# Kernel optimization log

Measured on AMD Instinct MI355X. Metric: run time of the kernel, lower is better.

Reference implementation:

```python
import jax, jax.numpy as jnp
import numpy as np


def _cdist(x, y):
    # Euclidean (p=2) pairwise distances, matching torch.cdist.
    # x: [B, N, D], y: [B, M, D] -> [B, N, M]
    xx = jnp.sum(x * x, axis=-1)                      # [B, N]
    yy = jnp.sum(y * y, axis=-1)                      # [B, M]
    zz = jnp.einsum('bnd,bmd->bnm', x, y)             # [B, N, M]
    d2 = xx[:, :, None] + yy[:, None, :] - 2.0 * zz
    return jnp.sqrt(jnp.maximum(d2, 0.0))


def setup_inputs() -> dict:
    key = jax.random.key(0)
    k1, k2 = jax.random.split(key)
    gts = jax.random.normal(k1, (4, 8192, 3), dtype=jnp.float32)
    preds = jax.random.normal(k2, (4, 8192, 3), dtype=jnp.float32)
    return {"gts": gts, "preds": preds}


def reference(gts, preds):
    P = _cdist(gts, preds)                 # [B, N, M]
    loss_1 = jnp.sum(jnp.min(P, axis=1), axis=1)  # min over gts points, sum over preds
    loss_2 = jnp.sum(jnp.min(P, axis=2), axis=1)  # min over preds points, sum over gts
    return loss_1 + loss_2                 # [B]
```

## Files before the change

kernel.cpp:

```cpp
#include <hip/hip_runtime.h>
#include <math.h>

#define BB 4
#define NPTS 8192
#define THREADS 512
#define NQ_TOTAL (2 * BB * NPTS)
#define QBLK 256
#define QPWV 32
#define CHUNK 2048
#define NCHUNK (NPTS / CHUNK)
#define NFRAG (CHUNK / 32)
#define GLDS_PER_WAVE (CHUNK / 8 / 64)
#define FBLK (2 * BB * (NPTS / QBLK))

typedef __attribute__((ext_vector_type(8)))  short bf16x8;
typedef __attribute__((ext_vector_type(16))) float f32x16;


__device__ __forceinline__ unsigned short f2bf(float f) {
    unsigned u = __float_as_uint(f);
    u += 0x7FFF + ((u >> 16) & 1);
    return (unsigned short)(u >> 16);
}
__device__ __forceinline__ float bf2f(unsigned short h) {
    return __uint_as_float(((unsigned)h) << 16);
}

__global__ __launch_bounds__(256) void pack_kernel(
    const float* __restrict__ gts, const float* __restrict__ preds,
    uint4* __restrict__ refpack, uint4* __restrict__ qpack,
    float* __restrict__ out) {
    int idx = blockIdx.x * 256 + threadIdx.x;
    if (idx < BB) out[idx] = 0.0f;
    if (idx >= NQ_TOTAL) return;
    int set  = idx / (BB * NPTS);
    int pidx = idx - set * (BB * NPTS);
    const float* src = set ? preds : gts;
    unsigned short hx = f2bf(src[pidx * 3 + 0]);
    unsigned short hy = f2bf(src[pidx * 3 + 1]);
    unsigned short hz = f2bf(src[pidx * 3 + 2]);
    float fx = bf2f(hx), fy = bf2f(hy), fz = bf2f(hz);
    float rr = fmaf(fx, fx, fmaf(fy, fy, fz * fz));
    unsigned short hrr = f2bf(rr);
    unsigned short hlo = f2bf(rr - bf2f(hrr));
    const unsigned short ONE = 0x3F80;

    uint4 rv;
    rv.x = (unsigned)hx  | ((unsigned)hy  << 16);
    rv.y = (unsigned)hz  | ((unsigned)hrr << 16);
    rv.z = (unsigned)hlo | ((unsigned)ONE << 16);
    rv.w = (unsigned)ONE;
    refpack[idx] = rv;

    unsigned short nx = f2bf(-2.0f * fx);
    unsigned short ny = f2bf(-2.0f * fy);
    unsigned short nz = f2bf(-2.0f * fz);
    uint4 qv;
    qv.x = (unsigned)nx  | ((unsigned)ny  << 16);
    qv.y = (unsigned)nz  | ((unsigned)ONE << 16);
    qv.z = (unsigned)ONE | ((unsigned)hrr << 16);
    qv.w = (unsigned)hlo;
    qpack[idx] = qv;
}

#define FOLD8(P)                                                   \
    c0 = fminf(fminf((P)[0],  (P)[1]),  c0);                       \
    c1 = fminf(fminf((P)[2],  (P)[3]),  c1);                       \
    c2 = fminf(fminf((P)[4],  (P)[5]),  c2);                       \
    c3 = fminf(fminf((P)[6],  (P)[7]),  c3);                       \
    c0 = fminf(fminf((P)[8],  (P)[9]),  c0);                       \
    c1 = fminf(fminf((P)[10], (P)[11]), c1);                       \
    c2 = fminf(fminf((P)[12], (P)[13]), c2);                       \
    c3 = fminf(fminf((P)[14], (P)[15]), c3);

#define STEP(AQ, FN, DO_LOAD)                                               \
    {                                                                       \
        f32x16 dn = __builtin_amdgcn_mfma_f32_32x32x16_bf16(AQ, bq, zc, 0, 0, 0); \
        if (DO_LOAD) AQ = sp[(FN) * 32 + l31];                              \
        FOLD8(pp);                                                          \
        pp = pc; pc = dn;                                                   \
    }

#define STAGE(BUF, CBASE)                                                   \
    _Pragma("unroll")                                                       \
    for (int i = 0; i < GLDS_PER_WAVE; ++i)                                 \
        __builtin_amdgcn_global_load_lds(                                   \
            (const unsigned*)(rgl + (CBASE) + wid * 256 + i * 64 + lane),   \
            (unsigned*)&sref[BUF][wid * 256 + i * 64], 16, 0, 0);

__global__ __launch_bounds__(THREADS, 2) void chamfer_kernel(
    const uint4* __restrict__ refpack, const uint4* __restrict__ qpack,
    float* __restrict__ out) {
    __shared__ uint4 sref[2][CHUNK];

    int tid  = threadIdx.x;
    int blk  = blockIdx.x;
    int dir  = blk >> 7;
    int b    = (blk >> 5) & 3;
    int qg   = blk & 31;
    int rset = dir;
    int qset = dir ^ 1;
    int wid  = tid >> 6;
    int lane = tid & 63;
    int l31  = lane & 31;

    const uint4* rgl = refpack + (size_t)(rset * BB + b) * NPTS;

    STAGE(0, 0);

    size_t qoff = (size_t)(qset * BB + b) * NPTS + (size_t)qg * QBLK
                + (size_t)wid * QPWV;
    bf16x8 bq = {0, 0, 0, 0, 0, 0, 0, 0};
    if (lane < 32) bq = ((const bf16x8*)qpack)[qoff + l31];
    __syncthreads();

    f32x16 zc;
    #pragma unroll
    for (int r = 0; r < 16; ++r) zc[r] = 0.0f;

    float c0 = 3.0e38f, c1 = 3.0e38f, c2 = 3.0e38f, c3 = 3.0e38f;

    for (int c = 0; c < NCHUNK; ++c) {
        if (c + 1 < NCHUNK) {
            STAGE((c + 1) & 1, (c + 1) * CHUNK);
        }

        const bf16x8* sp = (const bf16x8*)sref[c & 1];

        bf16x8 a0 = sp[0 * 32 + l31];
        bf16x8 a1 = sp[1 * 32 + l31];
        bf16x8 a2 = sp[2 * 32 + l31];
        bf16x8 a3 = sp[3 * 32 + l31];
        bf16x8 a4 = sp[4 * 32 + l31];
        bf16x8 a5 = sp[5 * 32 + l31];
        bf16x8 a6 = sp[6 * 32 + l31];
        bf16x8 a7 = sp[7 * 32 + l31];

        f32x16 pp, pc;
        #pragma unroll
        for (int r = 0; r < 16; ++r) { pp[r] = 3.0e38f; pc[r] = 3.0e38f; }

        #pragma unroll
        for (int m = 0; m < NFRAG / 8; ++m) {
            const bool L = (m < NFRAG / 8 - 1);
            STEP(a0, (m + 1) * 8 + 0, L);
            STEP(a1, (m + 1) * 8 + 1, L);
            STEP(a2, (m + 1) * 8 + 2, L);
            STEP(a3, (m + 1) * 8 + 3, L);
            STEP(a4, (m + 1) * 8 + 4, L);
            STEP(a5, (m + 1) * 8 + 5, L);
            STEP(a6, (m + 1) * 8 + 6, L);
            STEP(a7, (m + 1) * 8 + 7, L);
        }
        FOLD8(pp);
        FOLD8(pc);

        __syncthreads();
    }

    float m = fminf(fminf(c0, c1), fminf(c2, c3));
    m = fminf(m, __shfl_xor(m, 32, 64));

    float d = 0.0f;
    if (lane < 32) d = sqrtf(fmaxf(m, 0.0f));
    #pragma unroll
    for (int off = 16; off > 0; off >>= 1)
        d += __shfl_down(d, off, 64);

    float* wsf = (float*)&sref[0][0];
    if (lane == 0) wsf[wid] = d;
    __syncthreads();
    if (tid == 0) {
        float s = wsf[0] + wsf[1] + wsf[2] + wsf[3]
                + wsf[4] + wsf[5] + wsf[6] + wsf[7];
        atomicAdd(out + b, s);
    }
}

extern "C" void kernel_launch(void* const* d_in, const int* in_sizes, int n_in,
                              void* d_out, int out_size, void* d_ws, size_t ws_size,
                              hipStream_t stream) {
    const float* gts   = (const float*)d_in[0];
    const float* preds = (const float*)d_in[1];
    float* out = (float*)d_out;

    char* ws = (char*)d_ws;
    uint4* refpack = (uint4*)ws;
    uint4* qpack   = (uint4*)(ws + (size_t)NQ_TOTAL * 16);

    pack_kernel<<<NQ_TOTAL / 256, 256, 0, stream>>>(
        gts, preds, refpack, qpack, out);

    chamfer_kernel<<<FBLK, THREADS, 0, stream>>>(refpack, qpack, out);
}
```

Before: 72.50 us.

## Split reference set in halves, double queries per wave, merge mins atomically

Each wave now handles 64 queries with two B fragments, so every A fragment loaded from LDS feeds two MFMAs, which halves the LDS reads per MFMA. The reference set is split into two halves across blocks, keeping the grid at 256 blocks. Partial minimum distances go to a workspace through atomicMin on the uint bit pattern, and a new merge kernel takes square roots and sums them. This costs an extra kernel launch, global atomics and more register pressure from the doubled accumulators.

```diff
diff --git a/kernel.cpp b/kernel.cpp
--- a/kernel.cpp
+++ b/kernel.cpp
@@ -5,13 +5,14 @@
 #define NPTS 8192
 #define THREADS 512
 #define NQ_TOTAL (2 * BB * NPTS)
-#define QBLK 256
-#define QPWV 32
+#define QBLK 512
+#define QPWV 64
+#define HALFN 4096
 #define CHUNK 2048
-#define NCHUNK (NPTS / CHUNK)
+#define NCHUNK (HALFN / CHUNK)
 #define NFRAG (CHUNK / 32)
 #define GLDS_PER_WAVE (CHUNK / 8 / 64)
-#define FBLK (2 * BB * (NPTS / QBLK))
+#define FBLK 256
 
 typedef __attribute__((ext_vector_type(8)))  short bf16x8;
 typedef __attribute__((ext_vector_type(16))) float f32x16;
@@ -29,10 +30,11 @@
 __global__ __launch_bounds__(256) void pack_kernel(
     const float* __restrict__ gts, const float* __restrict__ preds,
     uint4* __restrict__ refpack, uint4* __restrict__ qpack,
-    float* __restrict__ out) {
+    unsigned* __restrict__ minpart, float* __restrict__ out) {
     int idx = blockIdx.x * 256 + threadIdx.x;
     if (idx < BB) out[idx] = 0.0f;
     if (idx >= NQ_TOTAL) return;
+    minpart[idx] = 0x7F7FFFFFu;
     int set  = idx / (BB * NPTS);
     int pidx = idx - set * (BB * NPTS);
     const float* src = set ? preds : gts;
@@ -63,22 +65,25 @@
     qpack[idx] = qv;
 }
 
-#define FOLD8(P)                                                   \
-    c0 = fminf(fminf((P)[0],  (P)[1]),  c0);                       \
-    c1 = fminf(fminf((P)[2],  (P)[3]),  c1);                       \
-    c2 = fminf(fminf((P)[4],  (P)[5]),  c2);                       \
-    c3 = fminf(fminf((P)[6],  (P)[7]),  c3);                       \
-    c0 = fminf(fminf((P)[8],  (P)[9]),  c0);                       \
-    c1 = fminf(fminf((P)[10], (P)[11]), c1);                       \
-    c2 = fminf(fminf((P)[12], (P)[13]), c2);                       \
-    c3 = fminf(fminf((P)[14], (P)[15]), c3);
-
-#define STEP(AQ, FN, DO_LOAD)                                               \
+#define FOLD8(P, X0, X1, X2, X3)                                   \
+    X0 = fminf(fminf((P)[0],  (P)[1]),  X0);                       \
+    X1 = fminf(fminf((P)[2],  (P)[3]),  X1);                       \
+    X2 = fminf(fminf((P)[4],  (P)[5]),  X2);                       \
+    X3 = fminf(fminf((P)[6],  (P)[7]),  X3);                       \
+    X0 = fminf(fminf((P)[8],  (P)[9]),  X0);                       \
+    X1 = fminf(fminf((P)[10], (P)[11]), X1);                       \
+    X2 = fminf(fminf((P)[12], (P)[13]), X2);                       \
+    X3 = fminf(fminf((P)[14], (P)[15]), X3);
+
+#define STEP2(AQ, FN, DO_LOAD)                                              \
     {                                                                       \
-        f32x16 dn = __builtin_amdgcn_mfma_f32_32x32x16_bf16(AQ, bq, zc, 0, 0, 0); \
+        f32x16 dn0 = __builtin_amdgcn_mfma_f32_32x32x16_bf16(AQ, bq0, zc, 0, 0, 0); \
+        f32x16 dn1 = __builtin_amdgcn_mfma_f32_32x32x16_bf16(AQ, bq1, zc, 0, 0, 0); \
         if (DO_LOAD) AQ = sp[(FN) * 32 + l31];                              \
-        FOLD8(pp);                                                          \
-        pp = pc; pc = dn;                                                   \
+        FOLD8(pp0, c0, c1, c2, c3);                                         \
+        FOLD8(pp1, c4, c5, c6, c7);                                         \
+        pp0 = pc0; pc0 = dn0;                                               \
+        pp1 = pc1; pc1 = dn1;                                               \
     }
 
 #define STAGE(BUF, CBASE)                                                   \
@@ -90,28 +95,34 @@
 
 __global__ __launch_bounds__(THREADS, 2) void chamfer_kernel(
     const uint4* __restrict__ refpack, const uint4* __restrict__ qpack,
-    float* __restrict__ out) {
+    unsigned* __restrict__ minpart) {
     __shared__ uint4 sref[2][CHUNK];
 
     int tid  = threadIdx.x;
     int blk  = blockIdx.x;
-    int dir  = blk >> 7;
-    int b    = (blk >> 5) & 3;
-    int qg   = blk & 31;
+    int half = blk >> 7;
+    int dir  = (blk >> 6) & 1;
+    int b    = (blk >> 4) & 3;
+    int qg   = blk & 15;
     int rset = dir;
     int qset = dir ^ 1;
     int wid  = tid >> 6;
     int lane = tid & 63;
     int l31  = lane & 31;
 
-    const uint4* rgl = refpack + (size_t)(rset * BB + b) * NPTS;
+    const uint4* rgl = refpack + (size_t)(rset * BB + b) * NPTS
+                     + (size_t)half * HALFN;
 
     STAGE(0, 0);
 
     size_t qoff = (size_t)(qset * BB + b) * NPTS + (size_t)qg * QBLK
                 + (size_t)wid * QPWV;
-    bf16x8 bq = {0, 0, 0, 0, 0, 0, 0, 0};
-    if (lane < 32) bq = ((const bf16x8*)qpack)[qoff + l31];
+    bf16x8 bq0 = {0, 0, 0, 0, 0, 0, 0, 0};
+    bf16x8 bq1 = {0, 0, 0, 0, 0, 0, 0, 0};
+    if (lane < 32) {
+        bq0 = ((const bf16x8*)qpack)[qoff + l31];
+        bq1 = ((const bf16x8*)qpack)[qoff + 32 + l31];
+    }
     __syncthreads();
 
     f32x16 zc;
@@ -119,6 +130,7 @@
     for (int r = 0; r < 16; ++r) zc[r] = 0.0f;
 
     float c0 = 3.0e38f, c1 = 3.0e38f, c2 = 3.0e38f, c3 = 3.0e38f;
+    float c4 = 3.0e38f, c5 = 3.0e38f, c6 = 3.0e38f, c7 = 3.0e38f;
 
     for (int c = 0; c < NCHUNK; ++c) {
         if (c + 1 < NCHUNK) {
@@ -136,45 +148,65 @@
         bf16x8 a6 = sp[6 * 32 + l31];
         bf16x8 a7 = sp[7 * 32 + l31];
 
-        f32x16 pp, pc;
+        f32x16 pp0, pc0, pp1, pc1;
         #pragma unroll
-        for (int r = 0; r < 16; ++r) { pp[r] = 3.0e38f; pc[r] = 3.0e38f; }
+        for (int r = 0; r < 16; ++r) {
+            pp0[r] = 3.0e38f; pc0[r] = 3.0e38f;
+            pp1[r] = 3.0e38f; pc1[r] = 3.0e38f;
+        }
 
         #pragma unroll
         for (int m = 0; m < NFRAG / 8; ++m) {
             const bool L = (m < NFRAG / 8 - 1);
-            STEP(a0, (m + 1) * 8 + 0, L);
-            STEP(a1, (m + 1) * 8 + 1, L);
-            STEP(a2, (m + 1) * 8 + 2, L);
-            STEP(a3, (m + 1) * 8 + 3, L);
-            STEP(a4, (m + 1) * 8 + 4, L);
-            STEP(a5, (m + 1) * 8 + 5, L);
-            STEP(a6, (m + 1) * 8 + 6, L);
-            STEP(a7, (m + 1) * 8 + 7, L);
+            STEP2(a0, (m + 1) * 8 + 0, L);
+            STEP2(a1, (m + 1) * 8 + 1, L);
+            STEP2(a2, (m + 1) * 8 + 2, L);
+            STEP2(a3, (m + 1) * 8 + 3, L);
+            STEP2(a4, (m + 1) * 8 + 4, L);
+            STEP2(a5, (m + 1) * 8 + 5, L);
+            STEP2(a6, (m + 1) * 8 + 6, L);
+            STEP2(a7, (m + 1) * 8 + 7, L);
         }
-        FOLD8(pp);
-        FOLD8(pc);
+        FOLD8(pp0, c0, c1, c2, c3);
+        FOLD8(pc0, c0, c1, c2, c3);
+        FOLD8(pp1, c4, c5, c6, c7);
+        FOLD8(pc1, c4, c5, c6, c7);
 
         __syncthreads();
     }
 
-    float m = fminf(fminf(c0, c1), fminf(c2, c3));
-    m = fminf(m, __shfl_xor(m, 32, 64));
-
-    float d = 0.0f;
-    if (lane < 32) d = sqrtf(fmaxf(m, 0.0f));
+    float m0 = fminf(fminf(c0, c1), fminf(c2, c3));
+    m0 = fminf(m0, __shfl_xor(m0, 32, 64));
+    float m1 = fminf(fminf(c4, c5), fminf(c6, c7));
+    m1 = fminf(m1, __shfl_xor(m1, 32, 64));
+
+    size_t qid = (size_t)(dir * BB + b) * NPTS + (size_t)qg * QBLK
+               + (size_t)wid * QPWV;
+    if (lane < 32) {
+        atomicMin(minpart + qid + l31,      __float_as_uint(fmaxf(m0, 0.0f)));
+        atomicMin(minpart + qid + 32 + l31, __float_as_uint(fmaxf(m1, 0.0f)));
+    }
+}
+
+__global__ __launch_bounds__(256) void merge_kernel(
+    const unsigned* __restrict__ minpart, float* __restrict__ out) {
+    int t  = blockIdx.x * 256 + threadIdx.x;
+    uint4 v = ((const uint4*)minpart)[t];
+    float d = sqrtf(__uint_as_float(v.x)) + sqrtf(__uint_as_float(v.y))
+            + sqrtf(__uint_as_float(v.z)) + sqrtf(__uint_as_float(v.w));
+    int b = (blockIdx.x >> 3) & 3;
+
     #pragma unroll
-    for (int off = 16; off > 0; off >>= 1)
+    for (int off = 32; off > 0; off >>= 1)
         d += __shfl_down(d, off, 64);
 
-    float* wsf = (float*)&sref[0][0];
-    if (lane == 0) wsf[wid] = d;
+    __shared__ float wsum[4];
+    int lane = threadIdx.x & 63;
+    int wid  = threadIdx.x >> 6;
+    if (lane == 0) wsum[wid] = d;
     __syncthreads();
-    if (tid == 0) {
-        float s = wsf[0] + wsf[1] + wsf[2] + wsf[3]
-                + wsf[4] + wsf[5] + wsf[6] + wsf[7];
-        atomicAdd(out + b, s);
-    }
+    if (threadIdx.x == 0)
+        atomicAdd(out + b, wsum[0] + wsum[1] + wsum[2] + wsum[3]);
 }
 
 extern "C" void kernel_launch(void* const* d_in, const int* in_sizes, int n_in,
@@ -185,11 +217,14 @@
     float* out = (float*)d_out;
 
     char* ws = (char*)d_ws;
-    uint4* refpack = (uint4*)ws;
-    uint4* qpack   = (uint4*)(ws + (size_t)NQ_TOTAL * 16);
+    uint4*    refpack = (uint4*)ws;
+    uint4*    qpack   = (uint4*)(ws + (size_t)NQ_TOTAL * 16);
+    unsigned* minpart = (unsigned*)(ws + (size_t)NQ_TOTAL * 32);
 
     pack_kernel<<<NQ_TOTAL / 256, 256, 0, stream>>>(
-        gts, preds, refpack, qpack, out);
-
-    chamfer_kernel<<<FBLK, THREADS, 0, stream>>>(refpack, qpack, out);
-}
+        gts, preds, refpack, qpack, minpart, out);
+
+    chamfer_kernel<<<FBLK, THREADS, 0, stream>>>(refpack, qpack, minpart);
+
+    merge_kernel<<<NQ_TOTAL / 4 / 256, 256, 0, stream>>>(minpart, out);
+}
```

New measurement: 72.49 us. No clear change (-0.0%).
